# Optimization experiments

Measured on AMD Instinct MI355X. Metric: run time of the kernel, lower is better.

## Reference

```python
import jax, jax.numpy as jnp
import numpy as np

B, STATE_DIM, ACTION_DIM = 16384, 512, 64
HID, NQ, QED = 1024, 64, 64
EPS = 1e-5


def _layernorm(x, gamma, beta):
    mu = jnp.mean(x, axis=-1, keepdims=True)
    var = jnp.mean(jnp.square(x - mu), axis=-1, keepdims=True)
    return (x - mu) * jax.lax.rsqrt(var + EPS) * gamma + beta


def setup_inputs() -> dict:
    key = jax.random.key(0)
    ks = jax.random.split(key, 12)
    s = 0.02  # small init scale for stable activations
    return {
        "state": jax.random.normal(ks[0], (B, STATE_DIM), jnp.float32),
        "action": jax.random.normal(ks[1], (B, ACTION_DIM), jnp.float32),
        "W1": jax.random.normal(ks[2], (STATE_DIM + ACTION_DIM, HID), jnp.float32) * s,
        "b1": jax.random.normal(ks[3], (HID,), jnp.float32) * s,
        "g1": jnp.ones((HID,), jnp.float32),
        "be1": jnp.zeros((HID,), jnp.float32),
        "W2": jax.random.normal(ks[4], (HID, HID), jnp.float32) * s,
        "b2": jax.random.normal(ks[5], (HID,), jnp.float32) * s,
        "g2": jnp.ones((HID,), jnp.float32),
        "be2": jnp.zeros((HID,), jnp.float32),
        "Wq1": jax.random.normal(ks[6], (1, QED), jnp.float32) * s,
        "bq1": jax.random.normal(ks[7], (QED,), jnp.float32) * s,
        "Wq2": jax.random.normal(ks[8], (QED, QED), jnp.float32) * s,
        "bq2": jax.random.normal(ks[9], (QED,), jnp.float32) * s,
        "Wh": jax.random.normal(ks[10], (HID + QED, 1), jnp.float32) * s,
        "bh": jax.random.normal(ks[11], (1,), jnp.float32) * s,
    }


def reference(state, action, W1, b1, g1, be1, W2, b2, g2, be2,
              Wq1, bq1, Wq2, bq2, Wh, bh):
    # tau buffer: midpoints of NQ uniform bins
    tau = jnp.linspace(0.0, 1.0, NQ + 1)[:-1] + 1.0 / (2 * NQ)  # [NQ]

    # feature_net (Dropout is identity in eval)
    x = jnp.concatenate([state, action], axis=-1)               # [B, S+A]
    h = jax.nn.relu(_layernorm(x @ W1 + b1, g1, be1))           # [B, HID]
    h = jax.nn.relu(_layernorm(h @ W2 + b2, g2, be2))           # [B, HID]

    # quantile embedding: tau rows are batch-independent -> one [NQ, QED] MLP
    te = jax.nn.relu(tau[:, None] @ Wq1 + bq1) @ Wq2 + bq2      # [NQ, QED]

    # head on concat([features, tau_emb]) == split the head weight
    Wf, Wt = Wh[:HID, 0], Wh[HID:, 0]                           # [HID], [QED]
    quantiles = h @ Wf[:, None] + (te @ Wt)[None, :] + bh[0]    # [B, NQ]
    return quantiles
```

## Files before the change

kernel.cpp:

```cpp
#include <hip/hip_runtime.h>
#include <hip/hip_bf16.h>
#include <cstddef>

#define B_ROWS 16384
#define SDIM 512
#define ADIM 64
#define KDIM 576
#define HID 1024
#define NQ 64

#define SEG0_ITEMS (B_ROWS * (SDIM / 8))
#define SEG1_ITEMS (B_ROWS * (ADIM / 8))
#define EW_ITEMS (SEG0_ITEMS + SEG1_ITEMS)
#define EW_BLOCKS 2048
#define T1_BLOCKS ((KDIM / 32) * (HID / 32))
#define T2_BLOCKS ((HID / 32) * (HID / 32))
#define PREP_BLOCKS (EW_BLOCKS + T1_BLOCKS + T2_BLOCKS + 1)

#define FK_LDS (16384 + 131072)

typedef __attribute__((ext_vector_type(8))) __bf16 bf16x8;
typedef __attribute__((ext_vector_type(4))) float f32x4;

static __device__ __forceinline__ float bf2f(unsigned short u) {
  union { unsigned int i; float f; } x; x.i = ((unsigned int)u) << 16; return x.f;
}
static __device__ __forceinline__ unsigned short f2bf(float f) {
  union { float f; unsigned int i; } x; x.f = f;
  unsigned int i = x.i + (0x7fffu + ((x.i >> 16) & 1u));
  return (unsigned short)(i >> 16);
}

static __device__ __forceinline__ void gload_lds16(const unsigned short* g, unsigned short* l) {
  __builtin_amdgcn_global_load_lds(
      (const __attribute__((address_space(1))) void*)(const void*)g,
      (__attribute__((address_space(3))) void*)(void*)l, 16, 0, 0);
}

static __device__ __forceinline__ ushort4 cvt8lo(float4 a) {
  ushort4 o; o.x = f2bf(a.x); o.y = f2bf(a.y); o.z = f2bf(a.z); o.w = f2bf(a.w);
  return o;
}

static __device__ __forceinline__ void transpose_body(
    const float* __restrict__ W, unsigned short* __restrict__ Wb,
    int Kin, int N, int k0, int n0, unsigned short* tile) {
  const int tx = threadIdx.x & 31, ty = threadIdx.x >> 5;
#pragma unroll
  for (int i = 0; i < 32; i += 8)
    tile[(ty + i) * 33 + tx] = f2bf(W[(size_t)(k0 + ty + i) * N + n0 + tx]);
  __syncthreads();
#pragma unroll
  for (int i = 0; i < 32; i += 8)
    Wb[(size_t)(n0 + ty + i) * Kin + k0 + tx] = tile[tx * 33 + ty + i];
}

__global__ __launch_bounds__(256) void prep_k(
    const float* __restrict__ state, const float* __restrict__ action,
    const float* __restrict__ W1, const float* __restrict__ W2,
    const float* __restrict__ Wq1, const float* __restrict__ bq1,
    const float* __restrict__ Wq2, const float* __restrict__ bq2,
    const float* __restrict__ Wh, const float* __restrict__ bh,
    unsigned short* __restrict__ xb, unsigned short* __restrict__ w1b,
    unsigned short* __restrict__ w2b, float* __restrict__ qoff) {
  __shared__ unsigned short tile[32 * 33];
  const int b = blockIdx.x;
  if (b < EW_BLOCKS) {
    for (int i = b * 256 + (int)threadIdx.x; i < EW_ITEMS; i += EW_BLOCKS * 256) {
      if (i < SEG0_ITEMS) {
        const int r = i >> 6, c = (i & 63) << 3;
        const float* sp = state + (size_t)r * SDIM + c;
        float4 a = *(const float4*)sp;
        float4 bb = *(const float4*)(sp + 4);
        unsigned short* yp = xb + (size_t)r * KDIM + c;
        *(ushort4*)yp = cvt8lo(a);
        *(ushort4*)(yp + 4) = cvt8lo(bb);
      } else {
        const int j = i - SEG0_ITEMS;
        const int r = j >> 3, ca = (j & 7) << 3;
        const float* ap = action + (size_t)r * ADIM + ca;
        float4 a = *(const float4*)ap;
        float4 bb = *(const float4*)(ap + 4);
        unsigned short* yp = xb + (size_t)r * KDIM + SDIM + ca;
        *(ushort4*)yp = cvt8lo(a);
        *(ushort4*)(yp + 4) = cvt8lo(bb);
      }
    }
  } else if (b < EW_BLOCKS + T1_BLOCKS) {
    const int t = b - EW_BLOCKS;
    transpose_body(W1, w1b, KDIM, HID, (t / 32) * 32, (t % 32) * 32, tile);
  } else if (b < EW_BLOCKS + T1_BLOCKS + T2_BLOCKS) {
    const int t = b - EW_BLOCKS - T1_BLOCKS;
    transpose_body(W2, w2b, HID, HID, (t / 32) * 32, (t % 32) * 32, tile);
  } else {
    const int q = threadIdx.x;
    if (q < NQ) {
      const float tau = ((float)q + 0.5f) * (1.0f / (float)NQ);
      float t1[64];
#pragma unroll
      for (int k = 0; k < 64; ++k) t1[k] = fmaxf(fmaf(tau, Wq1[k], bq1[k]), 0.f);
      float acc = bh[0];
#pragma unroll 1
      for (int j = 0; j < 64; ++j) {
        float t2 = bq2[j];
#pragma unroll
        for (int k = 0; k < 64; ++k) t2 = fmaf(t1[k], Wq2[k * 64 + j], t2);
        acc = fmaf(t2, Wh[HID + j], acc);
      }
      qoff[q] = acc;
    }
  }
}

template <bool FINAL>
__global__ __launch_bounds__(512, 2) void fused_k(
    const unsigned short* __restrict__ A,
    const unsigned short* __restrict__ Bt,
    const float* __restrict__ bias, const float* __restrict__ g,
    const float* __restrict__ be, const float* __restrict__ Wh,
    const float* __restrict__ qoff,
    unsigned short* __restrict__ Hout, float* __restrict__ Qout,
    int K, int NT) {
  extern __shared__ unsigned short sm[];
  __shared__ float part[8][64][2];
  __shared__ float murs[64][2];
  __shared__ float dotf[64];
  __shared__ float qof[64];

  const int tid = threadIdx.x;
  const int w = tid >> 6, l = tid & 63;
  const int r0 = (int)blockIdx.x * 64;
  const int sb = (int)blockIdx.x % NT;

  const int sce = ((((l & 7) << 4) ^ (((l >> 3) & 4) << 3)) >> 1);
  const int lr = (l & 15) << 7;
  const int cSw = (((l >> 4) << 4) ^ ((l & 4) << 3));

  f32x4 acc[4][8] = {};

#define KT(x) ((((x) + sb) % NT) << 6)
#define AF(d, mi, kk) (*(const bf16x8*)(sm + (((d)*8192 + (mi)*2048 + lr + cSw + ((kk) << 6)) >> 1)))
#define BFW(ni, kk) (*(const bf16x8*)(sm + ((16384 + w*16384 + (ni)*2048 + lr + cSw + ((kk) << 6)) >> 1)))
#define ISSUE_A(d, kt) \
    gload_lds16(A + (size_t)(r0 + w * 8 + (l >> 3)) * K + (kt) + sce, \
                sm + (((d)*8192 + w * 1024) >> 1))
#define ISSUE_B(kt) do { _Pragma("unroll") for (int i_ = 0; i_ < 16; ++i_) \
    gload_lds16(Bt + (size_t)(w * 128 + i_ * 8 + (l >> 3)) * K + (kt) + sce, \
                sm + ((16384 + w * 16384 + i_ * 1024) >> 1)); } while (0)
#define BAR() __builtin_amdgcn_s_barrier()
#define WAITLGKM() asm volatile("s_waitcnt lgkmcnt(0)" ::: "memory")
#define WAITVM(n) asm volatile("s_waitcnt vmcnt(" #n ")" ::: "memory")

  ISSUE_A(0, KT(0));
  ISSUE_B(KT(0));
  ISSUE_A(1, KT(1));
  WAITVM(17); BAR();

  for (int t = 0; t < NT; ++t) {
    const int d = t & 1;
    if (t + 1 < NT) { WAITVM(1); } else { WAITVM(0); }
    bf16x8 af[4], bfr[8];
#pragma unroll
    for (int mi = 0; mi < 4; ++mi) af[mi] = AF(d, mi, 0);
#pragma unroll
    for (int ni = 0; ni < 8; ++ni) bfr[ni] = BFW(ni, 0);
    __builtin_amdgcn_s_setprio(1);
#pragma unroll
    for (int mi = 0; mi < 4; ++mi)
#pragma unroll
      for (int ni = 0; ni < 8; ++ni)
        acc[mi][ni] = __builtin_amdgcn_mfma_f32_16x16x32_bf16(af[mi], bfr[ni], acc[mi][ni], 0, 0, 0);
    __builtin_amdgcn_s_setprio(0);
#pragma unroll
    for (int mi = 0; mi < 4; ++mi) af[mi] = AF(d, mi, 1);
#pragma unroll
    for (int ni = 0; ni < 8; ++ni) bfr[ni] = BFW(ni, 1);
    WAITLGKM();
    if (t + 1 < NT) ISSUE_B(KT(t + 1));
    __builtin_amdgcn_s_setprio(1);
#pragma unroll
    for (int mi = 0; mi < 4; ++mi)
#pragma unroll
      for (int ni = 0; ni < 8; ++ni)
        acc[mi][ni] = __builtin_amdgcn_mfma_f32_16x16x32_bf16(af[mi], bfr[ni], acc[mi][ni], 0, 0, 0);
    __builtin_amdgcn_s_setprio(0);
    if (t + 1 < NT) { WAITVM(16); }
    BAR();
    if (t + 2 < NT) ISSUE_A(d, KT(t + 2));
  }

  float bcol[8], gcol[8], becol[8];
#pragma unroll
  for (int ni = 0; ni < 8; ++ni) {
    const int col = w * 128 + ni * 16 + (l & 15);
    bcol[ni] = bias[col];
    gcol[ni] = g[col];
    becol[ni] = be[col];
  }
#pragma unroll
  for (int mi = 0; mi < 4; ++mi)
#pragma unroll
    for (int rr = 0; rr < 4; ++rr) {
      float s1 = 0.f, s2 = 0.f;
#pragma unroll
      for (int ni = 0; ni < 8; ++ni) {
        const float x = acc[mi][ni][rr] + bcol[ni];
        s1 += x; s2 += x * x;
      }
#pragma unroll
      for (int o = 1; o < 16; o <<= 1) {
        s1 += __shfl_xor(s1, o, 64);
        s2 += __shfl_xor(s2, o, 64);
      }
      if ((l & 15) == 0) {
        const int row = mi * 16 + (l >> 4) * 4 + rr;
        part[w][row][0] = s1;
        part[w][row][1] = s2;
      }
    }
  __syncthreads();
  if (tid < 64) {
    float s1 = 0.f, s2 = 0.f;
#pragma unroll
    for (int ww = 0; ww < 8; ++ww) { s1 += part[ww][tid][0]; s2 += part[ww][tid][1]; }
    const float mu = s1 * (1.0f / HID);
    murs[tid][0] = mu;
    murs[tid][1] = rsqrtf(s2 * (1.0f / HID) - mu * mu + 1e-5f);
    if (FINAL) qof[tid] = qoff[tid];
  }
  __syncthreads();

  if (!FINAL) {
#pragma unroll
    for (int mi = 0; mi < 4; ++mi)
#pragma unroll
      for (int rr = 0; rr < 4; ++rr) {
        const int row = mi * 16 + (l >> 4) * 4 + rr;
        const float mu = murs[row][0], rs = murs[row][1];
        unsigned short* hp = Hout + (size_t)(r0 + row) * HID + w * 128 + (l & 15);
#pragma unroll
        for (int ni = 0; ni < 8; ++ni) {
          const float x = acc[mi][ni][rr] + bcol[ni];
          hp[ni * 16] = f2bf(fmaxf((x - mu) * rs * gcol[ni] + becol[ni], 0.f));
        }
      }
  } else {
    float wf[8];
#pragma unroll
    for (int ni = 0; ni < 8; ++ni) wf[ni] = Wh[w * 128 + ni * 16 + (l & 15)];
#pragma unroll
    for (int mi = 0; mi < 4; ++mi)
#pragma unroll
      for (int rr = 0; rr < 4; ++rr) {
        const int row = mi * 16 + (l >> 4) * 4 + rr;
        const float mu = murs[row][0], rs = murs[row][1];
        float dp = 0.f;
#pragma unroll
        for (int ni = 0; ni < 8; ++ni) {
          const float x = acc[mi][ni][rr] + bcol[ni];
          dp += fmaxf((x - mu) * rs * gcol[ni] + becol[ni], 0.f) * wf[ni];
        }
#pragma unroll
        for (int o = 1; o < 16; o <<= 1) dp += __shfl_xor(dp, o, 64);
        if ((l & 15) == 0) part[w][row][0] = dp;
      }
    __syncthreads();
    if (tid < 64) {
      float dsum = 0.f;
#pragma unroll
      for (int ww = 0; ww < 8; ++ww) dsum += part[ww][tid][0];
      dotf[tid] = dsum;
    }
    __syncthreads();
#pragma unroll
    for (int it = 0; it < 8; ++it) {
      const int idx = tid + it * 512;
      const int row = idx >> 6, q = idx & 63;
      Qout[(size_t)(r0 + row) * NQ + q] = dotf[row] + qof[q];
    }
  }
#undef KT
#undef AF
#undef BFW
#undef ISSUE_A
#undef ISSUE_B
#undef BAR
#undef WAITLGKM
#undef WAITVM
}

extern "C" void kernel_launch(void* const* d_in, const int* in_sizes, int n_in,
                              void* d_out, int out_size, void* d_ws, size_t ws_size,
                              hipStream_t stream) {
  const float* state  = (const float*)d_in[0];
  const float* action = (const float*)d_in[1];
  const float* W1  = (const float*)d_in[2];
  const float* b1  = (const float*)d_in[3];
  const float* g1  = (const float*)d_in[4];
  const float* be1 = (const float*)d_in[5];
  const float* W2  = (const float*)d_in[6];
  const float* b2  = (const float*)d_in[7];
  const float* g2  = (const float*)d_in[8];
  const float* be2 = (const float*)d_in[9];
  const float* Wq1 = (const float*)d_in[10];
  const float* bq1 = (const float*)d_in[11];
  const float* Wq2 = (const float*)d_in[12];
  const float* bq2 = (const float*)d_in[13];
  const float* Wh  = (const float*)d_in[14];
  const float* bh  = (const float*)d_in[15];
  float* out = (float*)d_out;

  char* ws = (char*)d_ws;
  size_t off = 0;
  float* qoff = (float*)(ws + off); off += 256;
  unsigned short* xb  = (unsigned short*)(ws + off); off += (size_t)B_ROWS * KDIM * 2;
  unsigned short* w1b = (unsigned short*)(ws + off); off += (size_t)HID * KDIM * 2;
  unsigned short* w2b = (unsigned short*)(ws + off); off += (size_t)HID * HID * 2;
  unsigned short* h1b = (unsigned short*)(ws + off);

  (void)hipFuncSetAttribute((const void*)fused_k<false>, hipFuncAttributeMaxDynamicSharedMemorySize, FK_LDS);
  (void)hipFuncSetAttribute((const void*)fused_k<true>, hipFuncAttributeMaxDynamicSharedMemorySize, FK_LDS);

  prep_k<<<PREP_BLOCKS, 256, 0, stream>>>(state, action, W1, W2, Wq1, bq1, Wq2, bq2,
                                          Wh, bh, xb, w1b, w2b, qoff);

  fused_k<false><<<B_ROWS / 64, 512, FK_LDS, stream>>>(
      xb, w1b, b1, g1, be1, nullptr, nullptr, h1b, nullptr, KDIM, KDIM / 64);
  fused_k<true><<<B_ROWS / 64, 512, FK_LDS, stream>>>(
      h1b, w2b, b2, g2, be2, Wh, qoff, nullptr, out, HID, HID / 64);
}
```

Baseline: 108.4 us.

## Fuse fp32-to-bf16 input conversion into first GEMM A-tile loads

```diff
diff --git a/kernel.cpp b/kernel.cpp
--- a/kernel.cpp
+++ b/kernel.cpp
@@ -9,13 +9,9 @@
 #define HID 1024
 #define NQ 64
 
-#define SEG0_ITEMS (B_ROWS * (SDIM / 8))
-#define SEG1_ITEMS (B_ROWS * (ADIM / 8))
-#define EW_ITEMS (SEG0_ITEMS + SEG1_ITEMS)
-#define EW_BLOCKS 2048
 #define T1_BLOCKS ((KDIM / 32) * (HID / 32))
 #define T2_BLOCKS ((HID / 32) * (HID / 32))
-#define PREP_BLOCKS (EW_BLOCKS + T1_BLOCKS + T2_BLOCKS + 1)
+#define PREP_BLOCKS (T1_BLOCKS + T2_BLOCKS + 1)
 
 #define FK_LDS (16384 + 131072)
 
@@ -37,8 +33,12 @@
       (__attribute__((address_space(3))) void*)(void*)l, 16, 0, 0);
 }
 
-static __device__ __forceinline__ ushort4 cvt8lo(float4 a) {
-  ushort4 o; o.x = f2bf(a.x); o.y = f2bf(a.y); o.z = f2bf(a.z); o.w = f2bf(a.w);
+static __device__ __forceinline__ uint4 pack8(float4 a, float4 b) {
+  uint4 o;
+  o.x = (unsigned)f2bf(a.x) | ((unsigned)f2bf(a.y) << 16);
+  o.y = (unsigned)f2bf(a.z) | ((unsigned)f2bf(a.w) << 16);
+  o.z = (unsigned)f2bf(b.x) | ((unsigned)f2bf(b.y) << 16);
+  o.w = (unsigned)f2bf(b.z) | ((unsigned)f2bf(b.w) << 16);
   return o;
 }
 
@@ -56,41 +56,18 @@
 }
 
 __global__ __launch_bounds__(256) void prep_k(
-    const float* __restrict__ state, const float* __restrict__ action,
     const float* __restrict__ W1, const float* __restrict__ W2,
     const float* __restrict__ Wq1, const float* __restrict__ bq1,
     const float* __restrict__ Wq2, const float* __restrict__ bq2,
     const float* __restrict__ Wh, const float* __restrict__ bh,
-    unsigned short* __restrict__ xb, unsigned short* __restrict__ w1b,
-    unsigned short* __restrict__ w2b, float* __restrict__ qoff) {
+    unsigned short* __restrict__ w1b, unsigned short* __restrict__ w2b,
+    float* __restrict__ qoff) {
   __shared__ unsigned short tile[32 * 33];
   const int b = blockIdx.x;
-  if (b < EW_BLOCKS) {
-    for (int i = b * 256 + (int)threadIdx.x; i < EW_ITEMS; i += EW_BLOCKS * 256) {
-      if (i < SEG0_ITEMS) {
-        const int r = i >> 6, c = (i & 63) << 3;
-        const float* sp = state + (size_t)r * SDIM + c;
-        float4 a = *(const float4*)sp;
-        float4 bb = *(const float4*)(sp + 4);
-        unsigned short* yp = xb + (size_t)r * KDIM + c;
-        *(ushort4*)yp = cvt8lo(a);
-        *(ushort4*)(yp + 4) = cvt8lo(bb);
-      } else {
-        const int j = i - SEG0_ITEMS;
-        const int r = j >> 3, ca = (j & 7) << 3;
-        const float* ap = action + (size_t)r * ADIM + ca;
-        float4 a = *(const float4*)ap;
-        float4 bb = *(const float4*)(ap + 4);
-        unsigned short* yp = xb + (size_t)r * KDIM + SDIM + ca;
-        *(ushort4*)yp = cvt8lo(a);
-        *(ushort4*)(yp + 4) = cvt8lo(bb);
-      }
-    }
-  } else if (b < EW_BLOCKS + T1_BLOCKS) {
-    const int t = b - EW_BLOCKS;
-    transpose_body(W1, w1b, KDIM, HID, (t / 32) * 32, (t % 32) * 32, tile);
-  } else if (b < EW_BLOCKS + T1_BLOCKS + T2_BLOCKS) {
-    const int t = b - EW_BLOCKS - T1_BLOCKS;
+  if (b < T1_BLOCKS) {
+    transpose_body(W1, w1b, KDIM, HID, (b / 32) * 32, (b % 32) * 32, tile);
+  } else if (b < T1_BLOCKS + T2_BLOCKS) {
+    const int t = b - T1_BLOCKS;
     transpose_body(W2, w2b, HID, HID, (t / 32) * 32, (t % 32) * 32, tile);
   } else {
     const int q = threadIdx.x;
@@ -112,8 +89,10 @@
   }
 }
 
-template <bool FINAL>
+template <bool XSRC, bool FINAL>
 __global__ __launch_bounds__(512, 2) void fused_k(
+    const float* __restrict__ Xs,
+    const float* __restrict__ Xa,
     const unsigned short* __restrict__ A,
     const unsigned short* __restrict__ Bt,
     const float* __restrict__ bias, const float* __restrict__ g,
@@ -137,6 +116,7 @@
   const int cSw = (((l >> 4) << 4) ^ ((l & 4) << 3));
 
   f32x4 acc[4][8] = {};
+  float4 ar0, ar1;
 
 #define KT(x) ((((x) + sb) % NT) << 6)
 #define AF(d, mi, kk) (*(const bf16x8*)(sm + (((d)*8192 + (mi)*2048 + lr + cSw + ((kk) << 6)) >> 1)))
@@ -144,6 +124,13 @@
 #define ISSUE_A(d, kt) \
     gload_lds16(A + (size_t)(r0 + w * 8 + (l >> 3)) * K + (kt) + sce, \
                 sm + (((d)*8192 + w * 1024) >> 1))
+#define ALOADX(kt) do { \
+    const int row_ = r0 + w * 8 + (l >> 3); \
+    if ((kt) < SDIM) { const float* p_ = Xs + (size_t)row_ * SDIM + (kt) + sce; \
+      ar0 = *(const float4*)p_; ar1 = *(const float4*)(p_ + 4); } \
+    else { const float* p_ = Xa + (size_t)row_ * ADIM + ((kt) - SDIM) + sce; \
+      ar0 = *(const float4*)p_; ar1 = *(const float4*)(p_ + 4); } } while (0)
+#define AWRX(d) (*(uint4*)(sm + (((d)*8192 + w * 1024 + l * 16) >> 1)) = pack8(ar0, ar1))
 #define ISSUE_B(kt) do { _Pragma("unroll") for (int i_ = 0; i_ < 16; ++i_) \
     gload_lds16(Bt + (size_t)(w * 128 + i_ * 8 + (l >> 3)) * K + (kt) + sce, \
                 sm + ((16384 + w * 16384 + i_ * 1024) >> 1)); } while (0)
@@ -151,14 +138,22 @@
 #define WAITLGKM() asm volatile("s_waitcnt lgkmcnt(0)" ::: "memory")
 #define WAITVM(n) asm volatile("s_waitcnt vmcnt(" #n ")" ::: "memory")
 
-  ISSUE_A(0, KT(0));
-  ISSUE_B(KT(0));
-  ISSUE_A(1, KT(1));
-  WAITVM(17); BAR();
+  if (XSRC) {
+    ALOADX(KT(0)); AWRX(0);
+    ISSUE_B(KT(0));
+    if (NT > 1) ALOADX(KT(1));
+    WAITLGKM(); BAR();
+  } else {
+    ISSUE_A(0, KT(0));
+    ISSUE_B(KT(0));
+    ISSUE_A(1, KT(1));
+    WAITVM(17); BAR();
+  }
 
   for (int t = 0; t < NT; ++t) {
     const int d = t & 1;
-    if (t + 1 < NT) { WAITVM(1); } else { WAITVM(0); }
+    if (t + 1 < NT) { if (XSRC) { WAITVM(2); } else { WAITVM(1); } }
+    else { WAITVM(0); }
     bf16x8 af[4], bfr[8];
 #pragma unroll
     for (int mi = 0; mi < 4; ++mi) af[mi] = AF(d, mi, 0);
@@ -177,6 +172,7 @@
     for (int ni = 0; ni < 8; ++ni) bfr[ni] = BFW(ni, 1);
     WAITLGKM();
     if (t + 1 < NT) ISSUE_B(KT(t + 1));
+    if (XSRC && t + 1 < NT) AWRX((t + 1) & 1);
     __builtin_amdgcn_s_setprio(1);
 #pragma unroll
     for (int mi = 0; mi < 4; ++mi)
@@ -184,9 +180,15 @@
       for (int ni = 0; ni < 8; ++ni)
         acc[mi][ni] = __builtin_amdgcn_mfma_f32_16x16x32_bf16(af[mi], bfr[ni], acc[mi][ni], 0, 0, 0);
     __builtin_amdgcn_s_setprio(0);
-    if (t + 1 < NT) { WAITVM(16); }
-    BAR();
-    if (t + 2 < NT) ISSUE_A(d, KT(t + 2));
+    if (XSRC) {
+      if (t + 1 < NT) { WAITLGKM(); }
+      BAR();
+      if (t + 2 < NT) ALOADX(KT(t + 2));
+    } else {
+      if (t + 1 < NT) { WAITVM(16); }
+      BAR();
+      if (t + 2 < NT) ISSUE_A(d, KT(t + 2));
+    }
   }
 
   float bcol[8], gcol[8], becol[8];
@@ -283,6 +285,8 @@
 #undef AF
 #undef BFW
 #undef ISSUE_A
+#undef ALOADX
+#undef AWRX
 #undef ISSUE_B
 #undef BAR
 #undef WAITLGKM
@@ -313,19 +317,20 @@
   char* ws = (char*)d_ws;
   size_t off = 0;
   float* qoff = (float*)(ws + off); off += 256;
-  unsigned short* xb  = (unsigned short*)(ws + off); off += (size_t)B_ROWS * KDIM * 2;
   unsigned short* w1b = (unsigned short*)(ws + off); off += (size_t)HID * KDIM * 2;
   unsigned short* w2b = (unsigned short*)(ws + off); off += (size_t)HID * HID * 2;
   unsigned short* h1b = (unsigned short*)(ws + off);
 
-  (void)hipFuncSetAttribute((const void*)fused_k<false>, hipFuncAttributeMaxDynamicSharedMemorySize, FK_LDS);
-  (void)hipFuncSetAttribute((const void*)fused_k<true>, hipFuncAttributeMaxDynamicSharedMemorySize, FK_LDS);
-
-  prep_k<<<PREP_BLOCKS, 256, 0, stream>>>(state, action, W1, W2, Wq1, bq1, Wq2, bq2,
-                                          Wh, bh, xb, w1b, w2b, qoff);
-
-  fused_k<false><<<B_ROWS / 64, 512, FK_LDS, stream>>>(
-      xb, w1b, b1, g1, be1, nullptr, nullptr, h1b, nullptr, KDIM, KDIM / 64);
-  fused_k<true><<<B_ROWS / 64, 512, FK_LDS, stream>>>(
-      h1b, w2b, b2, g2, be2, Wh, qoff, nullptr, out, HID, HID / 64);
-}
+  (void)hipFuncSetAttribute((const void*)fused_k<true, false>, hipFuncAttributeMaxDynamicSharedMemorySize, FK_LDS);
+  (void)hipFuncSetAttribute((const void*)fused_k<false, true>, hipFuncAttributeMaxDynamicSharedMemorySize, FK_LDS);
+
+  prep_k<<<PREP_BLOCKS, 256, 0, stream>>>(W1, W2, Wq1, bq1, Wq2, bq2, Wh, bh,
+                                          w1b, w2b, qoff);
+
+  fused_k<true, false><<<B_ROWS / 64, 512, FK_LDS, stream>>>(
+      state, action, nullptr, w1b, b1, g1, be1, nullptr, nullptr,
+      h1b, nullptr, KDIM, KDIM / 64);
+  fused_k<false, true><<<B_ROWS / 64, 512, FK_LDS, stream>>>(
+      nullptr, nullptr, h1b, w2b, b2, g2, be2, Wh, qoff,
+      nullptr, out, HID, HID / 64);
+}
```

Result: no change. 107.8 us (-0.6%).
